# Optimization experiments

Measured on AMD Instinct MI355X. Metric: run time of the kernel, lower is better.

The kernel has to match this reference:

```python
import jax, jax.numpy as jnp
import numpy as np

L = 2048
LEVEL = 4
B = 16
D = 32

# pywt 'db4' decomposition filters (dec_lo, dec_hi), hardcoded to avoid pywt dep
DB4_DEC_LO = np.array([
    -0.010597401784997278, 0.032883011666982945, 0.030841381835986965,
    -0.18703481171888114, -0.02798376941698385, 0.6308807679295904,
    0.7148465705525415, 0.23037781330885523])
DB4_DEC_HI = np.array([
    -0.23037781330885523, 0.7148465705525415, -0.6308807679295904,
    -0.02798376941698385, 0.18703481171888114, 0.030841381835986965,
    -0.032883011666982945, -0.010597401784997278])


def _wavelet_dec_filter(vec, length, level):
    # filter[j][t][(t - 2^j * i) mod L] = vec[i]  (vectorized over t, i)
    wl = len(vec)
    f = np.zeros((level, length, length), dtype=np.float32)
    t = np.arange(length)[:, None]
    i = np.arange(wl)[None, :]
    rows = np.broadcast_to(t, (length, wl))
    for j in range(level):
        idx = (t - (2 ** j) * i) % length  # (L, wl)
        f[j, rows, idx] = vec[None, :]
    return f


def setup_inputs() -> dict:
    key = jax.random.key(0)
    x = jax.random.normal(key, (B, L, D), dtype=jnp.float32)
    h = DB4_DEC_HI / np.sqrt(2.0)
    g = DB4_DEC_LO / np.sqrt(2.0)
    w_dec_filter = jnp.asarray(_wavelet_dec_filter(h, L, LEVEL))  # (J, L, L)
    v_dec_filter = jnp.asarray(_wavelet_dec_filter(g, L, LEVEL))  # (J, L, L)
    return {"x": x, "w_dec_filter": w_dec_filter, "v_dec_filter": v_dec_filter}


def reference(x, w_dec_filter, v_dec_filter):
    # MODWT: x (B, L, D) -> wavecoeff (B, D, L, level+1)
    xt = jnp.transpose(x, (0, 2, 1))  # (B, D, L)
    level = w_dec_filter.shape[0]
    v_j = xt
    vs = []
    for j in range(level):  # sequential over small fixed number of levels
        v_j = jnp.einsum('ml,bdl->bdm', v_dec_filter[j], v_j)
        vs.append(v_j)
    v = jnp.stack(vs, axis=2)  # (B, D, J, L)
    # inputs to each detail filter: [x, v_0, ..., v_{J-2}]
    v_prime = jnp.concatenate([xt[:, :, None, :], v[:, :, :-1, :]], axis=2)  # (B, D, J, L)
    w = jnp.einsum('jml,bdjl->bdjm', w_dec_filter, v_prime)  # (B, D, J, L)
    wavecoeff = jnp.concatenate([w, v[:, :, -1:, :]], axis=2)  # (B, D, J+1, L)
    return jnp.transpose(wavecoeff, (0, 1, 3, 2))  # (B, D, L, J+1)
```

## Files before the change

kernel.cpp:

```cpp
#include <hip/hip_runtime.h>

#define L_LEN 2048
#define N_D   32
#define BLOCK 256
#define TILE  64
#define HALO  105
#define ROWS  (TILE + HALO)
#define LSTR  ROWS

__device__ __constant__ float G_[8] = {
    (float)(-0.010597401784997278 / 1.4142135623730951),
    (float)( 0.032883011666982945 / 1.4142135623730951),
    (float)( 0.030841381835986965 / 1.4142135623730951),
    (float)(-0.18703481171888114  / 1.4142135623730951),
    (float)(-0.02798376941698385  / 1.4142135623730951),
    (float)( 0.6308807679295904   / 1.4142135623730951),
    (float)( 0.7148465705525415   / 1.4142135623730951),
    (float)( 0.23037781330885523  / 1.4142135623730951)};
__device__ __constant__ float H_[8] = {
    (float)(-0.23037781330885523  / 1.4142135623730951),
    (float)( 0.7148465705525415   / 1.4142135623730951),
    (float)(-0.6308807679295904   / 1.4142135623730951),
    (float)(-0.02798376941698385  / 1.4142135623730951),
    (float)( 0.18703481171888114  / 1.4142135623730951),
    (float)( 0.030841381835986965 / 1.4142135623730951),
    (float)(-0.032883011666982945 / 1.4142135623730951),
    (float)(-0.010597401784997278 / 1.4142135623730951)};

template <int RANGE, int PMIN, int DIL, int CH, bool VLDS, bool VOUT>
__device__ __forceinline__ void level_pass(const float* __restrict__ src,
                                           float* __restrict__ dst,
                                           float* __restrict__ ob, int t) {
    for (int idx = t; idx < N_D * RANGE; idx += BLOCK) {
        const int d = idx / RANGE;
        const int p = PMIN + (idx - d * RANGE);
        const float* s = src + d * LSTR + p;
        float w = 0.f, v = 0.f;
#pragma unroll
        for (int i = 0; i < 8; ++i) {
            const float sv = s[-DIL * i];
            w = fmaf(H_[i], sv, w);
            v = fmaf(G_[i], sv, v);
        }
        if (VLDS) dst[d * LSTR + p] = v;
        if (p >= HALO) {
            float* o = ob + ((size_t)d * L_LEN + (p - HALO)) * 5;
            o[CH] = w;
            if (VOUT) o[4] = v;
        }
    }
}

__global__ __launch_bounds__(BLOCK) void swt_db4_kernel(const float* __restrict__ x,
                                                        float* __restrict__ out) {
    __shared__ float bufA[N_D * LSTR];
    __shared__ float bufB[N_D * LSTR];

    const int t  = threadIdx.x;
    const int b  = blockIdx.x >> 5;
    const int m0 = (blockIdx.x & 31) * TILE;

    const float* xb = x + (size_t)b * (L_LEN * N_D);
    float* ob = out + (((size_t)b * N_D) * L_LEN + m0) * 5;

    for (int idx = t; idx < N_D * ROWS; idx += BLOCK) {
        const int p  = idx >> 5;
        const int d  = idx & 31;
        const int gm = (m0 + p - HALO) & (L_LEN - 1);
        bufA[d * LSTR + p] = xb[(size_t)gm * N_D + d];
    }
    __syncthreads();

    level_pass<162,   7, 1, 0, true,  false>(bufA, bufB, ob, t);
    __syncthreads();
    level_pass<148,  21, 2, 1, true,  false>(bufB, bufA, ob, t);
    __syncthreads();
    level_pass<120,  49, 4, 2, true,  false>(bufA, bufB, ob, t);
    __syncthreads();
    level_pass< 64, 105, 8, 3, false, true >(bufB, bufA, ob, t);
}

extern "C" void kernel_launch(void* const* d_in, const int* in_sizes, int n_in,
                              void* d_out, int out_size, void* d_ws, size_t ws_size,
                              hipStream_t stream) {
    const float* x = (const float*)d_in[0];
    float* out = (float*)d_out;

    swt_db4_kernel<<<16 * 32, BLOCK, 0, stream>>>(x, out);
}
```

Before: 138.8 us.

## Register-block four outputs per thread, split channels across blocks, widen tile

Each thread now computes four outputs per level that share an 11-sample register window, which cuts redundant shared-memory loads. The tile along L doubles to 128 and each block handles 16 of the 32 channels, which lowers halo overhead per output while keeping the grid at 512 blocks. The filter coefficients become constexpr immediates instead of constant-memory loads. The trade-offs are more registers per thread and fewer active threads per pass (up to 912 work items for 256 threads), plus a padded shared buffer that absorbs the reads past the end of the window.

```diff
diff --git a/kernel.cpp b/kernel.cpp
--- a/kernel.cpp
+++ b/kernel.cpp
@@ -2,13 +2,16 @@
 
 #define L_LEN 2048
 #define N_D   32
+#define DSPL  16
 #define BLOCK 256
-#define TILE  64
+#define TILE  128
 #define HALO  105
 #define ROWS  (TILE + HALO)
 #define LSTR  ROWS
+#define LPAD  64
+#define BUFSZ (DSPL * LSTR + LPAD)
 
-__device__ __constant__ float G_[8] = {
+constexpr float G_[8] = {
     (float)(-0.010597401784997278 / 1.4142135623730951),
     (float)( 0.032883011666982945 / 1.4142135623730951),
     (float)( 0.030841381835986965 / 1.4142135623730951),
@@ -17,7 +20,7 @@
     (float)( 0.6308807679295904   / 1.4142135623730951),
     (float)( 0.7148465705525415   / 1.4142135623730951),
     (float)( 0.23037781330885523  / 1.4142135623730951)};
-__device__ __constant__ float H_[8] = {
+constexpr float H_[8] = {
     (float)(-0.23037781330885523  / 1.4142135623730951),
     (float)( 0.7148465705525415   / 1.4142135623730951),
     (float)(-0.6308807679295904   / 1.4142135623730951),
@@ -27,57 +30,75 @@
     (float)(-0.032883011666982945 / 1.4142135623730951),
     (float)(-0.010597401784997278 / 1.4142135623730951)};
 
-template <int RANGE, int PMIN, int DIL, int CH, bool VLDS, bool VOUT>
+template <int R, int PMIN, int LOG2D, int TPD, int CH, bool VLDS, bool VOUT>
 __device__ __forceinline__ void level_pass(const float* __restrict__ src,
                                            float* __restrict__ dst,
                                            float* __restrict__ ob, int t) {
-    for (int idx = t; idx < N_D * RANGE; idx += BLOCK) {
-        const int d = idx / RANGE;
-        const int p = PMIN + (idx - d * RANGE);
-        const float* s = src + d * LSTR + p;
-        float w = 0.f, v = 0.f;
+    constexpr int D = 1 << LOG2D;
+    for (int u = t; u < DSPL * TPD; u += BLOCK) {
+        const int d   = u / TPD;
+        const int j   = u - d * TPD;
+        const int off = j & (D - 1);
+        const int blk = j >> LOG2D;
+        const int p0  = PMIN + blk * (4 * D) + off;
+
+        const float* s = src + d * LSTR + (p0 - 7 * D);
+        float smp[11];
 #pragma unroll
-        for (int i = 0; i < 8; ++i) {
-            const float sv = s[-DIL * i];
-            w = fmaf(H_[i], sv, w);
-            v = fmaf(G_[i], sv, v);
-        }
-        if (VLDS) dst[d * LSTR + p] = v;
-        if (p >= HALO) {
-            float* o = ob + ((size_t)d * L_LEN + (p - HALO)) * 5;
-            o[CH] = w;
-            if (VOUT) o[4] = v;
+        for (int k = 0; k < 11; ++k) smp[k] = s[k * D];
+
+        float* db = dst + d * LSTR;
+        float* og = ob + (size_t)d * (L_LEN * 5);
+#pragma unroll
+        for (int r = 0; r < 4; ++r) {
+            const int p = p0 + r * D;
+            float w = 0.f, v = 0.f;
+#pragma unroll
+            for (int i = 0; i < 8; ++i) {
+                w = fmaf(H_[i], smp[7 + r - i], w);
+                v = fmaf(G_[i], smp[7 + r - i], v);
+            }
+            const bool valid = (p < ROWS);
+            if (VLDS && valid) db[p] = v;
+            if (valid && p >= HALO) {
+                float* o = og + (size_t)(p - HALO) * 5;
+                o[CH] = w;
+                if (VOUT) o[4] = v;
+            }
         }
     }
 }
 
 __global__ __launch_bounds__(BLOCK) void swt_db4_kernel(const float* __restrict__ x,
                                                         float* __restrict__ out) {
-    __shared__ float bufA[N_D * LSTR];
-    __shared__ float bufB[N_D * LSTR];
+    __shared__ float bufA[BUFSZ];
+    __shared__ float bufB[BUFSZ];
 
-    const int t  = threadIdx.x;
-    const int b  = blockIdx.x >> 5;
-    const int m0 = (blockIdx.x & 31) * TILE;
+    const int t    = threadIdx.x;
+    const int bid  = blockIdx.x;
+    const int dg   = bid & 1;
+    const int tile = (bid >> 1) & 15;
+    const int b    = bid >> 5;
+    const int m0   = tile * TILE;
 
-    const float* xb = x + (size_t)b * (L_LEN * N_D);
-    float* ob = out + (((size_t)b * N_D) * L_LEN + m0) * 5;
+    const float* xb = x + (size_t)b * (L_LEN * N_D) + dg * DSPL;
+    float* ob = out + (((size_t)b * N_D + dg * DSPL) * L_LEN + m0) * 5;
 
-    for (int idx = t; idx < N_D * ROWS; idx += BLOCK) {
-        const int p  = idx >> 5;
-        const int d  = idx & 31;
+    for (int idx = t; idx < DSPL * ROWS; idx += BLOCK) {
+        const int p  = idx >> 4;
+        const int d  = idx & 15;
         const int gm = (m0 + p - HALO) & (L_LEN - 1);
         bufA[d * LSTR + p] = xb[(size_t)gm * N_D + d];
     }
     __syncthreads();
 
-    level_pass<162,   7, 1, 0, true,  false>(bufA, bufB, ob, t);
+    level_pass<226,   7, 0, 57, 0, true,  false>(bufA, bufB, ob, t);
     __syncthreads();
-    level_pass<148,  21, 2, 1, true,  false>(bufB, bufA, ob, t);
+    level_pass<212,  21, 1, 54, 1, true,  false>(bufB, bufA, ob, t);
     __syncthreads();
-    level_pass<120,  49, 4, 2, true,  false>(bufA, bufB, ob, t);
+    level_pass<184,  49, 2, 48, 2, true,  false>(bufA, bufB, ob, t);
     __syncthreads();
-    level_pass< 64, 105, 8, 3, false, true >(bufB, bufA, ob, t);
+    level_pass<128, 105, 3, 32, 3, false, true >(bufB, bufA, ob, t);
 }
 
 extern "C" void kernel_launch(void* const* d_in, const int* in_sizes, int n_in,
@@ -86,5 +107,5 @@
     const float* x = (const float*)d_in[0];
     float* out = (float*)d_out;
 
-    swt_db4_kernel<<<16 * 32, BLOCK, 0, stream>>>(x, out);
+    swt_db4_kernel<<<16 * 16 * 2, BLOCK, 0, stream>>>(x, out);
 }
```

Result: slower. 144.5 us (+4.1%).
